# Kernel optimization log

Hardware: AMD Instinct MI355X
Metric: run time of the kernel (lower is better)

The kernel has to match this reference:

```python
import jax, jax.numpy as jnp
import numpy as np

ALPHA = 0.4
STEPS = 4
EPSILON = 0.005

N_NODES = 4096
N_EDGES = 131072
D_FEAT = 128


def setup_inputs() -> dict:
    key = jax.random.key(0)
    k1, k2, k3, k4 = jax.random.split(key, 4)
    x = jax.random.normal(k1, (N_NODES, D_FEAT), dtype=jnp.float32)
    src = jax.random.randint(k2, (N_EDGES,), 0, N_NODES)
    dst = jax.random.randint(k3, (N_EDGES,), 0, N_NODES)
    edge_index = jnp.stack([src, dst], axis=0).astype(jnp.int64)
    edge_attr = jax.random.uniform(k4, (N_EDGES,), dtype=jnp.float32)
    return {"x": x, "edge_index": edge_index, "edge_attr": edge_attr}


def reference(x, edge_index, edge_attr):
    # PPR power series: result = sum_i theta_i * A_i, where
    #   A_0 = edge pattern with unit values, A_1 = A (edge_attr),
    #   A_{i+1} = threshold_eps(A @ A_i).
    # Dense [N,N] representation: thresholding (dropping entries < eps in the
    # sparse original) is exactly zeroing those entries here; jit-compatible
    # since sparse nnz is data-dependent.
    N = x.shape[0]
    src, dst = edge_index[0], edge_index[1]
    A = jnp.zeros((N, N), dtype=edge_attr.dtype).at[src, dst].add(edge_attr)
    P0 = jnp.zeros((N, N), dtype=edge_attr.dtype).at[src, dst].add(1.0)

    mats = [P0, A]
    for _ in range(1, STEPS - 1):
        M = A @ mats[-1]
        M = jnp.where(M >= EPSILON, M, jnp.zeros((), dtype=M.dtype))
        mats.append(M)

    thetas = [ALPHA * (1.0 - ALPHA) ** i for i in range(STEPS)]
    out = thetas[0] * mats[0]
    for t, m in zip(thetas[1:], mats[1:]):
        out = out + t * m
    return out
```

## Files before the change

kernel.cpp:

```cpp
#include <hip/hip_runtime.h>

#define N_NODES 4096
#define EPS 0.005f
#define TH0 0.4f
#define TH1 0.24f
#define TH2 0.144f
#define TH3 0.0864f
#define JTILE 512
#define NTILES (N_NODES / JTILE)


static __device__ __forceinline__ float bf2f(unsigned short u) {
    union { unsigned int i; float f; } x;
    x.i = ((unsigned int)u) << 16;
    return x.f;
}

static __device__ __forceinline__ unsigned short f2bf(float f) {
    union { float f; unsigned int i; } x;
    x.f = f;
    unsigned int r = x.i + 0x7fff + ((x.i >> 16) & 1u);
    return (unsigned short)(r >> 16);
}

__global__ void hist_kernel(const int* __restrict__ idx, int E,
                            int* __restrict__ counts) {
    int e = blockIdx.x * blockDim.x + threadIdx.x;
    if (e < E) atomicAdd(&counts[idx[e]], 1);
}

__global__ __launch_bounds__(1024)
void scan_kernel(const int* __restrict__ counts, int* __restrict__ row_ptr,
                 int* __restrict__ cursor) {
    __shared__ int lds[1024];
    int t = threadIdx.x;
    int c0 = counts[4 * t + 0];
    int c1 = counts[4 * t + 1];
    int c2 = counts[4 * t + 2];
    int c3 = counts[4 * t + 3];
    int s = c0 + c1 + c2 + c3;
    lds[t] = s;
    __syncthreads();
    for (int off = 1; off < 1024; off <<= 1) {
        int v = 0;
        if (t >= off) v = lds[t - off];
        __syncthreads();
        lds[t] += v;
        __syncthreads();
    }
    int incl = lds[t];
    int base = incl - s;
    int r0 = base;
    int r1 = base + c0;
    int r2 = r1 + c1;
    int r3 = r2 + c2;
    row_ptr[4 * t + 0] = r0;  cursor[4 * t + 0] = r0;
    row_ptr[4 * t + 1] = r1;  cursor[4 * t + 1] = r1;
    row_ptr[4 * t + 2] = r2;  cursor[4 * t + 2] = r2;
    row_ptr[4 * t + 3] = r3;  cursor[4 * t + 3] = r3;
    if (t == 1023) row_ptr[N_NODES] = incl;
}

__global__ void scatter_kernel(const int* __restrict__ idx,
                               const float* __restrict__ attr, int E,
                               int* __restrict__ cursor, int* __restrict__ col,
                               float* __restrict__ val) {
    int e = blockIdx.x * blockDim.x + threadIdx.x;
    if (e < E) {
        int s = idx[e];
        int d = idx[e + E];
        int pos = atomicAdd(&cursor[s], 1);
        col[pos] = d;
        val[pos] = attr[e];
    }
}

__global__ __launch_bounds__(256)
void m2_kernel(const int* __restrict__ row_ptr, const int* __restrict__ col,
               const float* __restrict__ val, unsigned short* __restrict__ m2) {
    __shared__ float acc[N_NODES];
    __shared__ int   kcol[64];
    __shared__ float kval[64];
    __shared__ int   kf0[64];
    __shared__ int   kf1[64];
    int i = blockIdx.x;
    int t = threadIdx.x;
    for (int j = t; j < N_NODES; j += 256) acc[j] = 0.0f;
    __syncthreads();
    int e0 = row_ptr[i], e1 = row_ptr[i + 1];
    int wave = t >> 6, lane = t & 63;
    for (int base = e0; base < e1; base += 64) {
        int n = min(64, e1 - base);
        if (t < n) {
            int k = col[base + t];
            kcol[t] = k;
            kval[t] = val[base + t];
            kf0[t] = row_ptr[k];
            kf1[t] = row_ptr[k + 1];
        }
        __syncthreads();
        for (int q = wave; q < n; q += 4) {
            float a = kval[q];
            int f1 = kf1[q];
            for (int f = kf0[q] + lane; f < f1; f += 64) {
                atomicAdd(&acc[col[f]], a * val[f]);
            }
        }
        __syncthreads();
    }
    size_t rb = (size_t)i * N_NODES;
    for (int j = t; j < N_NODES; j += 256) {
        float v = acc[j];
        m2[rb + j] = (v >= EPS) ? f2bf(v) : (unsigned short)0;
    }
}

__global__ __launch_bounds__(128)
void out_kernel(const int* __restrict__ row_ptr, const int* __restrict__ col,
                const float* __restrict__ val,
                const unsigned short* __restrict__ m2,
                float* __restrict__ out) {
    __shared__ float ap[JTILE];
    __shared__ int   kcol[128];
    __shared__ float kval[128];
    int i = blockIdx.x;
    int jb = blockIdx.y * JTILE;
    int t = threadIdx.x;
    for (int j = t; j < JTILE; j += 128) ap[j] = 0.0f;
    __syncthreads();
    int e0 = row_ptr[i], e1 = row_ptr[i + 1];
    float4 acc = make_float4(0.f, 0.f, 0.f, 0.f);
    for (int base = e0; base < e1; base += 128) {
        int n = min(128, e1 - base);
        if (t < n) {
            int c = col[base + t];
            float v = val[base + t];
            kcol[t] = c;
            kval[t] = v;
            int cl = c - jb;
            if ((unsigned)cl < (unsigned)JTILE)
                atomicAdd(&ap[cl], TH0 + TH1 * v);
        }
        __syncthreads();
        for (int q = 0; q < n; q++) {
            int k = kcol[q];
            float a = kval[q];
            const ushort4* r = (const ushort4*)(m2 + (size_t)k * N_NODES + jb);
            ushort4 u = r[t];
            acc.x = fmaf(a, bf2f(u.x), acc.x);
            acc.y = fmaf(a, bf2f(u.y), acc.y);
            acc.z = fmaf(a, bf2f(u.z), acc.z);
            acc.w = fmaf(a, bf2f(u.w), acc.w);
        }
        __syncthreads();
    }
    const ushort4* mi = (const ushort4*)(m2 + (size_t)i * N_NODES + jb);
    ushort4 um = mi[t];
    const float4* apv = (const float4*)ap;
    float4 p = apv[t];
    float4 res;
    res.x = p.x + TH2 * bf2f(um.x) + TH3 * ((acc.x >= EPS) ? acc.x : 0.0f);
    res.y = p.y + TH2 * bf2f(um.y) + TH3 * ((acc.y >= EPS) ? acc.y : 0.0f);
    res.z = p.z + TH2 * bf2f(um.z) + TH3 * ((acc.z >= EPS) ? acc.z : 0.0f);
    res.w = p.w + TH2 * bf2f(um.w) + TH3 * ((acc.w >= EPS) ? acc.w : 0.0f);
    ((float4*)(out + (size_t)i * N_NODES + jb))[t] = res;
}

extern "C" void kernel_launch(void* const* d_in, const int* in_sizes, int n_in,
                              void* d_out, int out_size, void* d_ws, size_t ws_size,
                              hipStream_t stream) {
    const int* idx = (const int*)d_in[1];
    const float* attr = (const float*)d_in[2];
    int E = in_sizes[1] / 2;

    char* ws = (char*)d_ws;
    int*   counts  = (int*)(ws);
    int*   row_ptr = (int*)(ws + (16 << 10));
    int*   cursor  = (int*)(ws + (48 << 10));
    int*   col     = (int*)(ws + (64 << 10));
    float* val     = (float*)(ws + (64 << 10) + (size_t)E * sizeof(int));
    unsigned short* m2 = (unsigned short*)(ws + (2 << 20));
    float* out     = (float*)d_out;

    hipMemsetAsync(counts, 0, N_NODES * sizeof(int), stream);
    hist_kernel<<<(E + 255) / 256, 256, 0, stream>>>(idx, E, counts);
    scan_kernel<<<1, 1024, 0, stream>>>(counts, row_ptr, cursor);
    scatter_kernel<<<(E + 255) / 256, 256, 0, stream>>>(idx, attr, E, cursor, col, val);
    m2_kernel<<<N_NODES, 256, 0, stream>>>(row_ptr, col, val, m2);
    out_kernel<<<dim3(N_NODES, NTILES), 128, 0, stream>>>(row_ptr, col, val, m2, out);
}
```

Before: 208.0 us.

## Pad atomic counters, use 8-lane groups in m2, batch loads in out kernel

Histogram and cursor counters are padded to one per 64-byte line so that atomics from different rows no longer contend on shared cache lines. The m2 kernel now assigns each neighbor row to an 8-thread group instead of a full 64-lane wave, matching the short average row length (~32 nnz) and keeping more lanes busy. The out kernel unrolls the neighbor loop by four, issuing four independent row loads before the FMAs, with zero-padded entries to cover the remainder. This costs a larger counter buffer and memset and a new workspace layout, and the padded entries read row 0 of m2.

```diff
diff --git a/kernel.cpp b/kernel.cpp
--- a/kernel.cpp
+++ b/kernel.cpp
@@ -8,6 +8,7 @@
 #define TH3 0.0864f
 #define JTILE 512
 #define NTILES (N_NODES / JTILE)
+#define CPAD 16
 
 
 static __device__ __forceinline__ float bf2f(unsigned short u) {
@@ -26,7 +27,7 @@
 __global__ void hist_kernel(const int* __restrict__ idx, int E,
                             int* __restrict__ counts) {
     int e = blockIdx.x * blockDim.x + threadIdx.x;
-    if (e < E) atomicAdd(&counts[idx[e]], 1);
+    if (e < E) atomicAdd(&counts[idx[e] * CPAD], 1);
 }
 
 __global__ __launch_bounds__(1024)
@@ -34,10 +35,10 @@
                  int* __restrict__ cursor) {
     __shared__ int lds[1024];
     int t = threadIdx.x;
-    int c0 = counts[4 * t + 0];
-    int c1 = counts[4 * t + 1];
-    int c2 = counts[4 * t + 2];
-    int c3 = counts[4 * t + 3];
+    int c0 = counts[(4 * t + 0) * CPAD];
+    int c1 = counts[(4 * t + 1) * CPAD];
+    int c2 = counts[(4 * t + 2) * CPAD];
+    int c3 = counts[(4 * t + 3) * CPAD];
     int s = c0 + c1 + c2 + c3;
     lds[t] = s;
     __syncthreads();
@@ -54,10 +55,10 @@
     int r1 = base + c0;
     int r2 = r1 + c1;
     int r3 = r2 + c2;
-    row_ptr[4 * t + 0] = r0;  cursor[4 * t + 0] = r0;
-    row_ptr[4 * t + 1] = r1;  cursor[4 * t + 1] = r1;
-    row_ptr[4 * t + 2] = r2;  cursor[4 * t + 2] = r2;
-    row_ptr[4 * t + 3] = r3;  cursor[4 * t + 3] = r3;
+    row_ptr[4 * t + 0] = r0;  cursor[(4 * t + 0) * CPAD] = r0;
+    row_ptr[4 * t + 1] = r1;  cursor[(4 * t + 1) * CPAD] = r1;
+    row_ptr[4 * t + 2] = r2;  cursor[(4 * t + 2) * CPAD] = r2;
+    row_ptr[4 * t + 3] = r3;  cursor[(4 * t + 3) * CPAD] = r3;
     if (t == 1023) row_ptr[N_NODES] = incl;
 }
 
@@ -69,7 +70,7 @@
     if (e < E) {
         int s = idx[e];
         int d = idx[e + E];
-        int pos = atomicAdd(&cursor[s], 1);
+        int pos = atomicAdd(&cursor[s * CPAD], 1);
         col[pos] = d;
         val[pos] = attr[e];
     }
@@ -88,7 +89,7 @@
     for (int j = t; j < N_NODES; j += 256) acc[j] = 0.0f;
     __syncthreads();
     int e0 = row_ptr[i], e1 = row_ptr[i + 1];
-    int wave = t >> 6, lane = t & 63;
+    int gid = t >> 3, gl = t & 7;
     for (int base = e0; base < e1; base += 64) {
         int n = min(64, e1 - base);
         if (t < n) {
@@ -99,10 +100,10 @@
             kf1[t] = row_ptr[k + 1];
         }
         __syncthreads();
-        for (int q = wave; q < n; q += 4) {
+        for (int q = gid; q < n; q += 32) {
             float a = kval[q];
             int f1 = kf1[q];
-            for (int f = kf0[q] + lane; f < f1; f += 64) {
+            for (int f = kf0[q] + gl; f < f1; f += 8) {
                 atomicAdd(&acc[col[f]], a * val[f]);
             }
         }
@@ -132,6 +133,7 @@
     float4 acc = make_float4(0.f, 0.f, 0.f, 0.f);
     for (int base = e0; base < e1; base += 128) {
         int n = min(128, e1 - base);
+        int n4 = (n + 3) & ~3;
         if (t < n) {
             int c = col[base + t];
             float v = val[base + t];
@@ -140,17 +142,36 @@
             int cl = c - jb;
             if ((unsigned)cl < (unsigned)JTILE)
                 atomicAdd(&ap[cl], TH0 + TH1 * v);
-        }
-        __syncthreads();
-        for (int q = 0; q < n; q++) {
-            int k = kcol[q];
-            float a = kval[q];
-            const ushort4* r = (const ushort4*)(m2 + (size_t)k * N_NODES + jb);
-            ushort4 u = r[t];
-            acc.x = fmaf(a, bf2f(u.x), acc.x);
-            acc.y = fmaf(a, bf2f(u.y), acc.y);
-            acc.z = fmaf(a, bf2f(u.z), acc.z);
-            acc.w = fmaf(a, bf2f(u.w), acc.w);
+        } else if (t < n4) {
+            kcol[t] = 0;
+            kval[t] = 0.0f;
+        }
+        __syncthreads();
+        for (int q = 0; q < n4; q += 4) {
+            int   k0 = kcol[q + 0]; float a0 = kval[q + 0];
+            int   k1 = kcol[q + 1]; float a1 = kval[q + 1];
+            int   k2 = kcol[q + 2]; float a2 = kval[q + 2];
+            int   k3 = kcol[q + 3]; float a3 = kval[q + 3];
+            ushort4 u0 = ((const ushort4*)(m2 + (size_t)k0 * N_NODES + jb))[t];
+            ushort4 u1 = ((const ushort4*)(m2 + (size_t)k1 * N_NODES + jb))[t];
+            ushort4 u2 = ((const ushort4*)(m2 + (size_t)k2 * N_NODES + jb))[t];
+            ushort4 u3 = ((const ushort4*)(m2 + (size_t)k3 * N_NODES + jb))[t];
+            acc.x = fmaf(a0, bf2f(u0.x), acc.x);
+            acc.y = fmaf(a0, bf2f(u0.y), acc.y);
+            acc.z = fmaf(a0, bf2f(u0.z), acc.z);
+            acc.w = fmaf(a0, bf2f(u0.w), acc.w);
+            acc.x = fmaf(a1, bf2f(u1.x), acc.x);
+            acc.y = fmaf(a1, bf2f(u1.y), acc.y);
+            acc.z = fmaf(a1, bf2f(u1.z), acc.z);
+            acc.w = fmaf(a1, bf2f(u1.w), acc.w);
+            acc.x = fmaf(a2, bf2f(u2.x), acc.x);
+            acc.y = fmaf(a2, bf2f(u2.y), acc.y);
+            acc.z = fmaf(a2, bf2f(u2.z), acc.z);
+            acc.w = fmaf(a2, bf2f(u2.w), acc.w);
+            acc.x = fmaf(a3, bf2f(u3.x), acc.x);
+            acc.y = fmaf(a3, bf2f(u3.y), acc.y);
+            acc.z = fmaf(a3, bf2f(u3.z), acc.z);
+            acc.w = fmaf(a3, bf2f(u3.w), acc.w);
         }
         __syncthreads();
     }
@@ -175,14 +196,14 @@
 
     char* ws = (char*)d_ws;
     int*   counts  = (int*)(ws);
-    int*   row_ptr = (int*)(ws + (16 << 10));
-    int*   cursor  = (int*)(ws + (48 << 10));
-    int*   col     = (int*)(ws + (64 << 10));
-    float* val     = (float*)(ws + (64 << 10) + (size_t)E * sizeof(int));
+    int*   cursor  = (int*)(ws + (256 << 10));
+    int*   row_ptr = (int*)(ws + (512 << 10));
+    int*   col     = (int*)(ws + (576 << 10));
+    float* val     = (float*)(ws + (1088 << 10));
     unsigned short* m2 = (unsigned short*)(ws + (2 << 20));
     float* out     = (float*)d_out;
 
-    hipMemsetAsync(counts, 0, N_NODES * sizeof(int), stream);
+    hipMemsetAsync(counts, 0, N_NODES * CPAD * sizeof(int), stream);
     hist_kernel<<<(E + 255) / 256, 256, 0, stream>>>(idx, E, counts);
     scan_kernel<<<1, 1024, 0, stream>>>(counts, row_ptr, cursor);
     scatter_kernel<<<(E + 255) / 256, 256, 0, stream>>>(idx, attr, E, cursor, col, val);
```

Measured after the change: 203.4 us. -2.2%, faster.

## Pad CSR rows to multiples of four and vectorize the edge gather loops

Applied to the files above, without the earlier changes.

Each CSR row is padded to a multiple of four edges; padding slots are zero-filled, and padding gets skipped through value checks. The output kernel can then read four edges at a time with wave-uniform readfirstlane indices, and drops the LDS staging and its barriers. Degree and cursor counters are spread out with a stride to cut atomic contention. The m2 kernel uses 8-lane groups per neighbour row, unsafe atomics and vectorized LDS clears and bf16 stores, and the output grid is linearized so the tiles of a row sit next to each other. The costs are extra memset traffic and the skipping of real edges whose weight is exactly zero.

```diff
diff --git a/kernel.cpp b/kernel.cpp
--- a/kernel.cpp
+++ b/kernel.cpp
@@ -8,6 +8,8 @@
 #define TH3 0.0864f
 #define JTILE 512
 #define NTILES (N_NODES / JTILE)
+#define CPAD 16
+#define EPADMAX (131072 + 4 * N_NODES)
 
 
 static __device__ __forceinline__ float bf2f(unsigned short u) {
@@ -26,19 +28,19 @@
 __global__ void hist_kernel(const int* __restrict__ idx, int E,
                             int* __restrict__ counts) {
     int e = blockIdx.x * blockDim.x + threadIdx.x;
-    if (e < E) atomicAdd(&counts[idx[e]], 1);
+    if (e < E) atomicAdd(&counts[idx[e] * CPAD], 1);
 }
 
 __global__ __launch_bounds__(1024)
-void scan_kernel(const int* __restrict__ counts, int* __restrict__ row_ptr,
+void scan_kernel(const int* __restrict__ counts, int* __restrict__ row4,
                  int* __restrict__ cursor) {
     __shared__ int lds[1024];
     int t = threadIdx.x;
-    int c0 = counts[4 * t + 0];
-    int c1 = counts[4 * t + 1];
-    int c2 = counts[4 * t + 2];
-    int c3 = counts[4 * t + 3];
-    int s = c0 + c1 + c2 + c3;
+    int p0 = (counts[(4 * t + 0) * CPAD] + 3) & ~3;
+    int p1 = (counts[(4 * t + 1) * CPAD] + 3) & ~3;
+    int p2 = (counts[(4 * t + 2) * CPAD] + 3) & ~3;
+    int p3 = (counts[(4 * t + 3) * CPAD] + 3) & ~3;
+    int s = p0 + p1 + p2 + p3;
     lds[t] = s;
     __syncthreads();
     for (int off = 1; off < 1024; off <<= 1) {
@@ -51,33 +53,33 @@
     int incl = lds[t];
     int base = incl - s;
     int r0 = base;
-    int r1 = base + c0;
-    int r2 = r1 + c1;
-    int r3 = r2 + c2;
-    row_ptr[4 * t + 0] = r0;  cursor[4 * t + 0] = r0;
-    row_ptr[4 * t + 1] = r1;  cursor[4 * t + 1] = r1;
-    row_ptr[4 * t + 2] = r2;  cursor[4 * t + 2] = r2;
-    row_ptr[4 * t + 3] = r3;  cursor[4 * t + 3] = r3;
-    if (t == 1023) row_ptr[N_NODES] = incl;
+    int r1 = base + p0;
+    int r2 = r1 + p1;
+    int r3 = r2 + p2;
+    row4[4 * t + 0] = r0;  cursor[(4 * t + 0) * CPAD] = r0;
+    row4[4 * t + 1] = r1;  cursor[(4 * t + 1) * CPAD] = r1;
+    row4[4 * t + 2] = r2;  cursor[(4 * t + 2) * CPAD] = r2;
+    row4[4 * t + 3] = r3;  cursor[(4 * t + 3) * CPAD] = r3;
+    if (t == 1023) row4[N_NODES] = incl;
 }
 
 __global__ void scatter_kernel(const int* __restrict__ idx,
                                const float* __restrict__ attr, int E,
-                               int* __restrict__ cursor, int* __restrict__ col,
-                               float* __restrict__ val) {
+                               int* __restrict__ cursor, int* __restrict__ col2,
+                               float* __restrict__ val2) {
     int e = blockIdx.x * blockDim.x + threadIdx.x;
     if (e < E) {
         int s = idx[e];
         int d = idx[e + E];
-        int pos = atomicAdd(&cursor[s], 1);
-        col[pos] = d;
-        val[pos] = attr[e];
+        int pos = atomicAdd(&cursor[s * CPAD], 1);
+        col2[pos] = d;
+        val2[pos] = attr[e];
     }
 }
 
 __global__ __launch_bounds__(256)
-void m2_kernel(const int* __restrict__ row_ptr, const int* __restrict__ col,
-               const float* __restrict__ val, unsigned short* __restrict__ m2) {
+void m2_kernel(const int* __restrict__ row4, const int* __restrict__ col2,
+               const float* __restrict__ val2, unsigned short* __restrict__ m2) {
     __shared__ float acc[N_NODES];
     __shared__ int   kcol[64];
     __shared__ float kval[64];
@@ -85,79 +87,99 @@
     __shared__ int   kf1[64];
     int i = blockIdx.x;
     int t = threadIdx.x;
-    for (int j = t; j < N_NODES; j += 256) acc[j] = 0.0f;
-    __syncthreads();
-    int e0 = row_ptr[i], e1 = row_ptr[i + 1];
-    int wave = t >> 6, lane = t & 63;
+    float4 z = make_float4(0.f, 0.f, 0.f, 0.f);
+    for (int j4 = t; j4 < N_NODES / 4; j4 += 256) ((float4*)acc)[j4] = z;
+    __syncthreads();
+    int e0 = row4[i], e1 = row4[i + 1];
+    int gid = t >> 3, gl = t & 7;
     for (int base = e0; base < e1; base += 64) {
         int n = min(64, e1 - base);
         if (t < n) {
-            int k = col[base + t];
+            int k = col2[base + t];
             kcol[t] = k;
-            kval[t] = val[base + t];
-            kf0[t] = row_ptr[k];
-            kf1[t] = row_ptr[k + 1];
+            kval[t] = val2[base + t];
+            kf0[t] = row4[k];
+            kf1[t] = row4[k + 1];
         }
         __syncthreads();
-        for (int q = wave; q < n; q += 4) {
+        for (int q = gid; q < n; q += 32) {
             float a = kval[q];
-            int f1 = kf1[q];
-            for (int f = kf0[q] + lane; f < f1; f += 64) {
-                atomicAdd(&acc[col[f]], a * val[f]);
+            if (a > 0.0f) {
+                int f1 = kf1[q];
+                for (int f = kf0[q] + gl; f < f1; f += 8) {
+                    unsafeAtomicAdd(&acc[col2[f]], a * val2[f]);
+                }
             }
         }
         __syncthreads();
     }
     size_t rb = (size_t)i * N_NODES;
-    for (int j = t; j < N_NODES; j += 256) {
-        float v = acc[j];
-        m2[rb + j] = (v >= EPS) ? f2bf(v) : (unsigned short)0;
+    for (int j4 = t; j4 < N_NODES / 4; j4 += 256) {
+        float4 v = ((const float4*)acc)[j4];
+        ushort4 r;
+        r.x = (v.x >= EPS) ? f2bf(v.x) : (unsigned short)0;
+        r.y = (v.y >= EPS) ? f2bf(v.y) : (unsigned short)0;
+        r.z = (v.z >= EPS) ? f2bf(v.z) : (unsigned short)0;
+        r.w = (v.w >= EPS) ? f2bf(v.w) : (unsigned short)0;
+        ((ushort4*)(m2 + rb))[j4] = r;
     }
 }
 
 __global__ __launch_bounds__(128)
-void out_kernel(const int* __restrict__ row_ptr, const int* __restrict__ col,
-                const float* __restrict__ val,
+void out_kernel(const int* __restrict__ row4, const int* __restrict__ col2,
+                const float* __restrict__ val2,
                 const unsigned short* __restrict__ m2,
                 float* __restrict__ out) {
     __shared__ float ap[JTILE];
-    __shared__ int   kcol[128];
-    __shared__ float kval[128];
-    int i = blockIdx.x;
-    int jb = blockIdx.y * JTILE;
+    int lin = blockIdx.x;
+    int tile = lin & 7;
+    int i = lin >> 3;
+    int jb = tile * JTILE;
     int t = threadIdx.x;
     for (int j = t; j < JTILE; j += 128) ap[j] = 0.0f;
     __syncthreads();
-    int e0 = row_ptr[i], e1 = row_ptr[i + 1];
+    int e0 = row4[i], e1 = row4[i + 1];
+    for (int e = e0 + t; e < e1; e += 128) {
+        float v = val2[e];
+        if (v > 0.0f) {
+            int cl = col2[e] - jb;
+            if ((unsigned)cl < (unsigned)JTILE)
+                unsafeAtomicAdd(&ap[cl], TH0 + TH1 * v);
+        }
+    }
     float4 acc = make_float4(0.f, 0.f, 0.f, 0.f);
-    for (int base = e0; base < e1; base += 128) {
-        int n = min(128, e1 - base);
-        if (t < n) {
-            int c = col[base + t];
-            float v = val[base + t];
-            kcol[t] = c;
-            kval[t] = v;
-            int cl = c - jb;
-            if ((unsigned)cl < (unsigned)JTILE)
-                atomicAdd(&ap[cl], TH0 + TH1 * v);
-        }
-        __syncthreads();
-        for (int q = 0; q < n; q++) {
-            int k = kcol[q];
-            float a = kval[q];
-            const ushort4* r = (const ushort4*)(m2 + (size_t)k * N_NODES + jb);
-            ushort4 u = r[t];
-            acc.x = fmaf(a, bf2f(u.x), acc.x);
-            acc.y = fmaf(a, bf2f(u.y), acc.y);
-            acc.z = fmaf(a, bf2f(u.z), acc.z);
-            acc.w = fmaf(a, bf2f(u.w), acc.w);
-        }
-        __syncthreads();
-    }
-    const ushort4* mi = (const ushort4*)(m2 + (size_t)i * N_NODES + jb);
-    ushort4 um = mi[t];
-    const float4* apv = (const float4*)ap;
-    float4 p = apv[t];
+    const unsigned short* m2t = m2 + jb + 4 * t;
+    for (int e = e0; e < e1; e += 4) {
+        int4   kq = *(const int4*)(col2 + e);
+        float4 aq = *(const float4*)(val2 + e);
+        int k0 = __builtin_amdgcn_readfirstlane(kq.x);
+        int k1 = __builtin_amdgcn_readfirstlane(kq.y);
+        int k2 = __builtin_amdgcn_readfirstlane(kq.z);
+        int k3 = __builtin_amdgcn_readfirstlane(kq.w);
+        ushort4 u0 = *(const ushort4*)(m2t + (size_t)k0 * N_NODES);
+        ushort4 u1 = *(const ushort4*)(m2t + (size_t)k1 * N_NODES);
+        ushort4 u2 = *(const ushort4*)(m2t + (size_t)k2 * N_NODES);
+        ushort4 u3 = *(const ushort4*)(m2t + (size_t)k3 * N_NODES);
+        acc.x = fmaf(aq.x, bf2f(u0.x), acc.x);
+        acc.y = fmaf(aq.x, bf2f(u0.y), acc.y);
+        acc.z = fmaf(aq.x, bf2f(u0.z), acc.z);
+        acc.w = fmaf(aq.x, bf2f(u0.w), acc.w);
+        acc.x = fmaf(aq.y, bf2f(u1.x), acc.x);
+        acc.y = fmaf(aq.y, bf2f(u1.y), acc.y);
+        acc.z = fmaf(aq.y, bf2f(u1.z), acc.z);
+        acc.w = fmaf(aq.y, bf2f(u1.w), acc.w);
+        acc.x = fmaf(aq.z, bf2f(u2.x), acc.x);
+        acc.y = fmaf(aq.z, bf2f(u2.y), acc.y);
+        acc.z = fmaf(aq.z, bf2f(u2.z), acc.z);
+        acc.w = fmaf(aq.z, bf2f(u2.w), acc.w);
+        acc.x = fmaf(aq.w, bf2f(u3.x), acc.x);
+        acc.y = fmaf(aq.w, bf2f(u3.y), acc.y);
+        acc.z = fmaf(aq.w, bf2f(u3.z), acc.z);
+        acc.w = fmaf(aq.w, bf2f(u3.w), acc.w);
+    }
+    __syncthreads();
+    ushort4 um = ((const ushort4*)(m2 + (size_t)i * N_NODES + jb))[t];
+    float4 p = ((const float4*)ap)[t];
     float4 res;
     res.x = p.x + TH2 * bf2f(um.x) + TH3 * ((acc.x >= EPS) ? acc.x : 0.0f);
     res.y = p.y + TH2 * bf2f(um.y) + TH3 * ((acc.y >= EPS) ? acc.y : 0.0f);
@@ -174,18 +196,19 @@
     int E = in_sizes[1] / 2;
 
     char* ws = (char*)d_ws;
-    int*   counts  = (int*)(ws);
-    int*   row_ptr = (int*)(ws + (16 << 10));
-    int*   cursor  = (int*)(ws + (48 << 10));
-    int*   col     = (int*)(ws + (64 << 10));
-    float* val     = (float*)(ws + (64 << 10) + (size_t)E * sizeof(int));
+    int*   counts = (int*)(ws);
+    int*   cursor = (int*)(ws + (256 << 10));
+    int*   row4   = (int*)(ws + (512 << 10));
+    int*   col2   = (int*)(ws + (576 << 10));
+    float* val2   = (float*)(ws + (1152 << 10));
     unsigned short* m2 = (unsigned short*)(ws + (2 << 20));
-    float* out     = (float*)d_out;
-
-    hipMemsetAsync(counts, 0, N_NODES * sizeof(int), stream);
+    float* out    = (float*)d_out;
+
+    hipMemsetAsync(counts, 0, N_NODES * CPAD * sizeof(int), stream);
+    hipMemsetAsync(col2, 0, 2 * EPADMAX * sizeof(int), stream);
     hist_kernel<<<(E + 255) / 256, 256, 0, stream>>>(idx, E, counts);
-    scan_kernel<<<1, 1024, 0, stream>>>(counts, row_ptr, cursor);
-    scatter_kernel<<<(E + 255) / 256, 256, 0, stream>>>(idx, attr, E, cursor, col, val);
-    m2_kernel<<<N_NODES, 256, 0, stream>>>(row_ptr, col, val, m2);
-    out_kernel<<<dim3(N_NODES, NTILES), 128, 0, stream>>>(row_ptr, col, val, m2, out);
-}
+    scan_kernel<<<1, 1024, 0, stream>>>(counts, row4, cursor);
+    scatter_kernel<<<(E + 255) / 256, 256, 0, stream>>>(idx, attr, E, cursor, col2, val2);
+    m2_kernel<<<N_NODES, 256, 0, stream>>>(row4, col2, val2, m2);
+    out_kernel<<<N_NODES * NTILES, 128, 0, stream>>>(row4, col2, val2, m2, out);
+}
```

After: 202.6 us. 2.6% less time.
